# Kernel tuning notes

Measured on AMD Instinct MI355X. Metric: run time of the kernel, lower is better.

Reference implementation:

```python
import jax, jax.numpy as jnp
import numpy as np

T, D, E = 8192, 1024, 64
CAPACITY_FACTOR = 2.0
CAP = int(CAPACITY_FACTOR * np.ceil(T / E))  # 256 (training-mode capacity)
EPS = 1e-4


def setup_inputs() -> dict:
    key = jax.random.key(0)
    k1, k2, k3 = jax.random.split(key, 3)
    x = jax.random.normal(k1, (T, D), dtype=jnp.float32)
    W_red = jax.random.normal(k2, (D, 4), dtype=jnp.float32) * 0.02
    centroids = jax.random.normal(k3, (E, 4), dtype=jnp.float32)
    return {"x": x, "W_red": W_red, "centroids": centroids}


def reference(x, W_red, centroids):
    # dim reduction (nn.Linear(model_dim, 4, bias=False))
    red = x @ W_red  # [T, 4]
    # cosine logits: centroids are L2-normalized inside _cosine (the in-place
    # 1.5/norm rescale of the parameter cancels under F.normalize)
    c = centroids.astype(jnp.float32)
    cn = c / jnp.maximum(jnp.linalg.norm(c, axis=1, keepdims=True), EPS)
    logits = red.astype(jnp.float32) @ cn.T  # [T, E]
    # _make_finite
    finite = jnp.isfinite(logits)
    fmin = jnp.min(jnp.where(finite, logits, jnp.inf))
    logits = jnp.where(finite, logits, fmin)

    gates = jax.nn.softmax(logits, axis=1)                 # [T, E]
    idx1 = jnp.argmax(gates, axis=1)                       # [T]
    mask1 = jax.nn.one_hot(idx1, E, dtype=gates.dtype)     # [T, E]
    expert_counts = jnp.sum(mask1, axis=0).astype(jnp.int32)  # metadata

    gates1_s = 1.5 * jnp.sum(gates * mask1, axis=1)        # [T]
    loc1 = jnp.cumsum(mask1, axis=0) - 1.0                 # positions within expert

    me = jnp.mean(gates, axis=0)
    ce = jnp.mean(mask1, axis=0)
    l_aux = jnp.mean(me * ce) * (E * E)

    mask1 = mask1 * (loc1 < CAP).astype(mask1.dtype)       # drop overflow tokens
    loc1_s = jnp.sum(loc1 * mask1, axis=1).astype(jnp.int32)  # [T]
    gates1 = gates1_s[:, None] * mask1                     # [T, E]
    loc_sc = jax.nn.one_hot(loc1_s, CAP, dtype=gates1.dtype)  # [T, CAP]
    combine = gates1[:, :, None] * loc_sc[:, None, :]      # [T, E, CAP]
    dispatch_mask = combine != 0
    return (l_aux, combine.astype(x.dtype), dispatch_mask, expert_counts)
```

## Files before the change

kernel.cpp:

```cpp
#include <hip/hip_runtime.h>

#define T 8192
#define D 1024
#define E 64
#define CAP 256

static const size_t TEC = (size_t)T * E * CAP;
#define C_OFF   ((size_t)1)
#define M_OFF   ((size_t)1 + (size_t)T * E * CAP)
#define CNT_OFF ((size_t)1 + 2 * (size_t)T * E * CAP)

__global__ __launch_bounds__(256) void k1_gate(
    const float* __restrict__ x, const float* __restrict__ Wred,
    const float* __restrict__ cent, int* __restrict__ idx1,
    float* __restrict__ g15, float* __restrict__ Sg)
{
    __shared__ float wcol[4 * D];
    __shared__ float cn[E * 4];
    __shared__ float sg[E];
    const int tid = threadIdx.x;

    for (int i = tid; i < 4 * D; i += 256) {
        int d = i >> 2, c = i & 3;
        wcol[c * D + d] = Wred[i];
    }
    if (tid < E) {
        float c0 = cent[tid * 4 + 0];
        float c1 = cent[tid * 4 + 1];
        float c2 = cent[tid * 4 + 2];
        float c3 = cent[tid * 4 + 3];
        float n = fmaxf(sqrtf(c0 * c0 + c1 * c1 + c2 * c2 + c3 * c3), 1e-4f);
        cn[tid * 4 + 0] = c0 / n;
        cn[tid * 4 + 1] = c1 / n;
        cn[tid * 4 + 2] = c2 / n;
        cn[tid * 4 + 3] = c3 / n;
        sg[tid] = 0.0f;
    }
    __syncthreads();

    const int wave = tid >> 6, lane = tid & 63;
    for (int it = 0; it < 4; ++it) {
        const int t = blockIdx.x * 16 + it * 4 + wave;
        const float* xr = x + (size_t)t * D;
        float a0 = 0.f, a1 = 0.f, a2 = 0.f, a3 = 0.f;
        #pragma unroll
        for (int k = 0; k < 16; ++k) {
            int d = k * 64 + lane;
            float xv = xr[d];
            a0 += xv * wcol[d];
            a1 += xv * wcol[D + d];
            a2 += xv * wcol[2 * D + d];
            a3 += xv * wcol[3 * D + d];
        }
        #pragma unroll
        for (int off = 32; off; off >>= 1) {
            a0 += __shfl_xor(a0, off);
            a1 += __shfl_xor(a1, off);
            a2 += __shfl_xor(a2, off);
            a3 += __shfl_xor(a3, off);
        }
        float logit = a0 * cn[lane * 4 + 0] + a1 * cn[lane * 4 + 1]
                    + a2 * cn[lane * 4 + 2] + a3 * cn[lane * 4 + 3];
        float m = logit;
        #pragma unroll
        for (int off = 32; off; off >>= 1) m = fmaxf(m, __shfl_xor(m, off));
        unsigned long long ball = __ballot(logit == m);
        int amax = __ffsll(ball) - 1;
        float ev = expf(logit - m);
        float s = ev;
        #pragma unroll
        for (int off = 32; off; off >>= 1) s += __shfl_xor(s, off);
        atomicAdd(&sg[lane], ev / s);
        if (lane == 0) { idx1[t] = amax; g15[t] = 1.5f / s; }
    }
    __syncthreads();
    if (tid < E) atomicAdd(&Sg[tid], sg[tid]);
}

__global__ __launch_bounds__(256) void k2_hist(const int* __restrict__ idx1,
                                               int* __restrict__ bc)
{
    __shared__ int h[E];
    const int tid = threadIdx.x;
    if (tid < E) h[tid] = 0;
    __syncthreads();
    atomicAdd(&h[idx1[blockIdx.x * 256 + tid]], 1);
    __syncthreads();
    if (tid < E) bc[blockIdx.x * E + tid] = h[tid];
}

__global__ __launch_bounds__(64) void k3_prefix(const int* __restrict__ bc,
                                                int* __restrict__ pf,
                                                const float* __restrict__ Sg,
                                                float* __restrict__ out)
{
    const int e = threadIdx.x;
    int run = 0;
    for (int b = 0; b < 32; ++b) {
        pf[b * E + e] = run;
        run += bc[b * E + e];
    }
    out[CNT_OFF + e] = (float)run;
    float v = Sg[e] * (float)run;
    #pragma unroll
    for (int off = 32; off; off >>= 1) v += __shfl_xor(v, off);
    if (e == 0) out[0] = v * ((float)E / ((float)T * (float)T));
}

__global__ __launch_bounds__(256) void k4_scatter(const int* __restrict__ idx1,
                                                  const float* __restrict__ g15,
                                                  const int* __restrict__ pf,
                                                  float* __restrict__ out)
{
    __shared__ int ids[256];
    const int tid = threadIdx.x;
    const int t = blockIdx.x * 256 + tid;
    const int e = idx1[t];
    ids[tid] = e;
    __syncthreads();
    int r = 0;
    for (int j = 0; j < 256; ++j)
        r += (j < tid && ids[j] == e) ? 1 : 0;
    const int rank = pf[blockIdx.x * E + e] + r;
    if (rank < CAP) {
        size_t off = (size_t)t * (E * CAP) + (size_t)e * CAP + rank;
        out[C_OFF + off] = g15[t];
        out[M_OFF + off] = 1.0f;
    }
}

extern "C" void kernel_launch(void* const* d_in, const int* in_sizes, int n_in,
                              void* d_out, int out_size, void* d_ws, size_t ws_size,
                              hipStream_t stream)
{
    const float* x    = (const float*)d_in[0];
    const float* Wred = (const float*)d_in[1];
    const float* cent = (const float*)d_in[2];
    float* out = (float*)d_out;

    char* ws = (char*)d_ws;
    int*   idx1 = (int*)ws;
    float* g15  = (float*)(ws + 32768);
    float* Sg   = (float*)(ws + 65536);
    int*   bc   = (int*)(ws + 65536 + 256);
    int*   pf   = (int*)(ws + 65536 + 256 + 8192);

    hipMemsetAsync(d_out, 0, (size_t)out_size, stream);
    hipMemsetAsync(Sg, 0, E * sizeof(float), stream);

    k1_gate<<<512, 256, 0, stream>>>(x, Wred, cent, idx1, g15, Sg);
    k2_hist<<<32, 256, 0, stream>>>(idx1, bc);
    k3_prefix<<<1, 64, 0, stream>>>(bc, pf, Sg, out);
    k4_scatter<<<32, 256, 0, stream>>>(idx1, g15, pf, out);
}
```

Before: 936.3 us.

## Fuse output zero-fill with scatter and fold histogram into gate kernel

Drops the full-output hipMemsetAsync and has a per-token kernel zero its own 16K-float combine and mask rows with vectorized nontemporal stores, then write the single nonzero entry. The per-chunk expert histogram moves into the gate kernel via global atomics, which removes the separate histogram launch. Within-chunk rank now comes from a ballot/popcount over the chunk instead of a serial 256-iteration loop. Memory traffic for the large output stays the same, but the fill is done by the kernel and is misaligned by one float, so it relies on peeled scalar edge stores.

New measurement: 1.163 ms. 24.2% more time.

```diff
diff --git a/kernel.cpp b/kernel.cpp
--- a/kernel.cpp
+++ b/kernel.cpp
@@ -4,6 +4,8 @@
 #define D 1024
 #define E 64
 #define CAP 256
+
+typedef float f32x4 __attribute__((ext_vector_type(4)));
 
 static const size_t TEC = (size_t)T * E * CAP;
 #define C_OFF   ((size_t)1)
@@ -13,7 +15,7 @@
 __global__ __launch_bounds__(256) void k1_gate(
     const float* __restrict__ x, const float* __restrict__ Wred,
     const float* __restrict__ cent, int* __restrict__ idx1,
-    float* __restrict__ g15, float* __restrict__ Sg)
+    float* __restrict__ g15, float* __restrict__ Sg, int* __restrict__ bc)
 {
     __shared__ float wcol[4 * D];
     __shared__ float cn[E * 4];
@@ -71,22 +73,14 @@
         #pragma unroll
         for (int off = 32; off; off >>= 1) s += __shfl_xor(s, off);
         atomicAdd(&sg[lane], ev / s);
-        if (lane == 0) { idx1[t] = amax; g15[t] = 1.5f / s; }
+        if (lane == 0) {
+            idx1[t] = amax;
+            g15[t] = 1.5f / s;
+            atomicAdd(&bc[(t >> 8) * E + amax], 1);
+        }
     }
     __syncthreads();
     if (tid < E) atomicAdd(&Sg[tid], sg[tid]);
-}
-
-__global__ __launch_bounds__(256) void k2_hist(const int* __restrict__ idx1,
-                                               int* __restrict__ bc)
-{
-    __shared__ int h[E];
-    const int tid = threadIdx.x;
-    if (tid < E) h[tid] = 0;
-    __syncthreads();
-    atomicAdd(&h[idx1[blockIdx.x * 256 + tid]], 1);
-    __syncthreads();
-    if (tid < E) bc[blockIdx.x * E + tid] = h[tid];
 }
 
 __global__ __launch_bounds__(64) void k3_prefix(const int* __restrict__ bc,
@@ -107,25 +101,46 @@
     if (e == 0) out[0] = v * ((float)E / ((float)T * (float)T));
 }
 
-__global__ __launch_bounds__(256) void k4_scatter(const int* __restrict__ idx1,
-                                                  const float* __restrict__ g15,
-                                                  const int* __restrict__ pf,
-                                                  float* __restrict__ out)
+__global__ __launch_bounds__(256) void k4_fill_scatter(
+    const int* __restrict__ idx1, const float* __restrict__ g15,
+    const int* __restrict__ pf, float* __restrict__ out)
 {
+    const int tid = threadIdx.x;
+    const int t = blockIdx.x;
+    const int chunk = t >> 8;
+    const int tin = t & 255;
+
     __shared__ int ids[256];
-    const int tid = threadIdx.x;
-    const int t = blockIdx.x * 256 + tid;
+    __shared__ int wsum[4];
     const int e = idx1[t];
-    ids[tid] = e;
+    ids[tid] = idx1[chunk * 256 + tid];
     __syncthreads();
-    int r = 0;
-    for (int j = 0; j < 256; ++j)
-        r += (j < tid && ids[j] == e) ? 1 : 0;
-    const int rank = pf[blockIdx.x * E + e] + r;
-    if (rank < CAP) {
-        size_t off = (size_t)t * (E * CAP) + (size_t)e * CAP + rank;
-        out[C_OFF + off] = g15[t];
-        out[M_OFF + off] = 1.0f;
+    int flag = (tid < tin && ids[tid] == e) ? 1 : 0;
+    unsigned long long b = __ballot(flag != 0);
+    if ((tid & 63) == 0) wsum[tid >> 6] = __popcll(b);
+    __syncthreads();
+    const int rank = pf[chunk * E + e] + wsum[0] + wsum[1] + wsum[2] + wsum[3];
+
+    float* __restrict__ crow = out + C_OFF + (size_t)t * (E * CAP);
+    float* __restrict__ mrow = out + M_OFF + (size_t)t * (E * CAP);
+    const f32x4 z4 = {0.f, 0.f, 0.f, 0.f};
+    #pragma unroll
+    for (int k = 0; k < 16; ++k) {
+        int i = tid + k * 256;
+        if (i < 4095) {
+            __builtin_nontemporal_store(z4, (f32x4*)(crow + 3 + 4 * (size_t)i));
+            __builtin_nontemporal_store(z4, (f32x4*)(mrow + 3 + 4 * (size_t)i));
+        }
+    }
+    if (tid == 0) {
+        crow[0] = 0.f; crow[1] = 0.f; crow[2] = 0.f; crow[16383] = 0.f;
+        mrow[0] = 0.f; mrow[1] = 0.f; mrow[2] = 0.f; mrow[16383] = 0.f;
+    }
+    __syncthreads();
+    if (tid == 0 && rank < CAP) {
+        size_t o = (size_t)e * CAP + rank;
+        crow[o] = g15[t];
+        mrow[o] = 1.0f;
     }
 }
 
@@ -145,11 +160,9 @@
     int*   bc   = (int*)(ws + 65536 + 256);
     int*   pf   = (int*)(ws + 65536 + 256 + 8192);
 
-    hipMemsetAsync(d_out, 0, (size_t)out_size, stream);
-    hipMemsetAsync(Sg, 0, E * sizeof(float), stream);
+    (void)hipMemsetAsync(Sg, 0, 256 + 32 * E * sizeof(int), stream);
 
-    k1_gate<<<512, 256, 0, stream>>>(x, Wred, cent, idx1, g15, Sg);
-    k2_hist<<<32, 256, 0, stream>>>(idx1, bc);
+    k1_gate<<<512, 256, 0, stream>>>(x, Wred, cent, idx1, g15, Sg, bc);
     k3_prefix<<<1, 64, 0, stream>>>(bc, pf, Sg, out);
-    k4_scatter<<<32, 256, 0, stream>>>(idx1, g15, pf, out);
+    k4_fill_scatter<<<T, 256, 0, stream>>>(idx1, g15, pf, out);
 }
```
